# Kernel optimization log

Measured on AMD Instinct MI355X. Metric: run time of the kernel, lower is better.

The kernel has to match this reference:

```python
import jax, jax.numpy as jnp
import numpy as np

DT = 0.01
STEPS = 30
D = 2048


def setup_inputs() -> dict:
    key = jax.random.key(0)
    ks = jax.random.split(key, 7)
    B, S = 4, 4096
    x = jax.random.normal(ks[0], (B, S, D), jnp.float32)
    lorenz = jnp.array([10.0, 28.0, 8.0 / 3.0], jnp.float32)
    strength = jnp.float32(0.3)
    W_in = jax.random.normal(ks[1], (3, D), jnp.float32) / np.sqrt(D)
    b_in = jax.random.normal(ks[2], (3,), jnp.float32) * 0.01
    W_out = jax.random.normal(ks[3], (D, 18), jnp.float32) / np.sqrt(18.0)
    b_out = jax.random.normal(ks[4], (D,), jnp.float32) * 0.01
    return {"x": x, "lorenz": lorenz, "strength": strength,
            "W_in": W_in, "b_in": b_in, "W_out": W_out, "b_out": b_out}


def _deriv(s, sigma, rho, beta):
    xx, yy, zz = s[..., 0], s[..., 1], s[..., 2]
    return jnp.stack([sigma * (yy - xx), xx * (rho - zz) - yy, xx * yy - beta * zz], axis=-1)


def reference(x, lorenz, strength, W_in, b_in, W_out, b_out):
    orig_shape = x.shape
    xf = x.reshape(-1, x.shape[-1])            # [N, D]
    state0 = xf @ W_in.T + b_in                # [N, 3]
    params = jnp.clip(jnp.abs(lorenz), 0.1, None)
    sigma, rho, beta = params[0], params[1], params[2]

    def step(s, _):
        k1 = _deriv(s, sigma, rho, beta)
        k2 = _deriv(s + 0.5 * DT * k1, sigma, rho, beta)
        k3 = _deriv(s + 0.5 * DT * k2, sigma, rho, beta)
        k4 = _deriv(s + DT * k3, sigma, rho, beta)
        s2 = s + (DT / 6.0) * (k1 + 2.0 * k2 + 2.0 * k3 + k4)
        return s2, s2

    _, ys = jax.lax.scan(step, state0, None, length=STEPS)  # [STEPS, N, 3]
    traj = jnp.concatenate([state0[:, None], jnp.moveaxis(ys, 0, 1)], axis=1)  # [N, STEPS+1, 3]

    feats = jnp.concatenate([
        traj[:, 0],                         # initial state
        traj[:, -1],                        # final state
        traj.mean(axis=1),
        traj.std(axis=1, ddof=1),           # torch.std is unbiased by default
        traj.min(axis=1),
        traj.max(axis=1),
    ], axis=-1)                             # [N, 18]

    pert = feats @ W_out.T + b_out          # [N, D]
    out = xf + jnp.tanh(pert) * jnp.abs(strength)
    return out.reshape(orig_shape)
```

## Files before the change

kernel.cpp:

```cpp
#include <hip/hip_runtime.h>
#include <math.h>

#define DD 2048
#define DTC 0.01f
#define NSTEPS 30

typedef float floatx4 __attribute__((ext_vector_type(4)));

__device__ __forceinline__ void lorenz_deriv(float x, float y, float z,
                                             float sigma, float rho, float beta,
                                             float& dx, float& dy, float& dz) {
    dx = sigma * (y - x);
    dy = x * (rho - z) - y;
    dz = x * y - beta * z;
}

__device__ __forceinline__ float fast_tanh(float p) {
    float e = __expf(2.0f * p);
    return 1.0f - __fdividef(2.0f, e + 1.0f);
}

__global__ __launch_bounds__(256) void kA_state0(
    const float* __restrict__ x, const float* __restrict__ W_in,
    const float* __restrict__ b_in, float* __restrict__ state0,
    const float* __restrict__ W_out, float* __restrict__ wsT) {
    __shared__ float g_lds[4][16][13];
    const int tid = threadIdx.x;
    const int lane = tid & 63;
    const int wv = tid >> 6;
    const int row0 = blockIdx.x * 4;
    const int c0 = tid * 8;

    floatx4 xr[4][2];
#pragma unroll
    for (int r = 0; r < 4; ++r) {
        const float* p = x + (size_t)(row0 + r) * DD + c0;
        xr[r][0] = *reinterpret_cast<const floatx4*>(p);
        xr[r][1] = *reinterpret_cast<const floatx4*>(p + 4);
    }
    floatx4 w[3][2];
#pragma unroll
    for (int k = 0; k < 3; ++k) {
        const float* p = W_in + (size_t)k * DD + c0;
        w[k][0] = *reinterpret_cast<const floatx4*>(p);
        w[k][1] = *reinterpret_cast<const floatx4*>(p + 4);
    }

    float s[12];
#pragma unroll
    for (int r = 0; r < 4; ++r) {
#pragma unroll
        for (int k = 0; k < 3; ++k) {
            floatx4 t = xr[r][0] * w[k][0] + xr[r][1] * w[k][1];
            s[r * 3 + k] = (t.x + t.y) + (t.z + t.w);
        }
    }

#pragma unroll
    for (int o = 0; o < 12; ++o) {
        s[o] += __shfl_xor(s[o], 32, 64);
        s[o] += __shfl_xor(s[o], 16, 64);
    }
    if (lane < 16) {
#pragma unroll
        for (int o = 0; o < 12; ++o) g_lds[wv][lane][o] = s[o];
    }
    __syncthreads();

    if (tid < 192) {
        const int o = tid >> 4;
        const int j = tid & 15;
        float v = g_lds[0][j][o] + g_lds[1][j][o] + g_lds[2][j][o] + g_lds[3][j][o];
#pragma unroll
        for (int off = 1; off < 16; off <<= 1) v += __shfl_xor(v, off, 64);
        if (j == 0) {
            state0[(size_t)(row0 + o / 3) * 3 + (o % 3)] = v + b_in[o % 3];
        }
    }

    if (blockIdx.x < 144) {
        const int oidx = blockIdx.x * 256 + tid;
        const int k = oidx >> 11;
        const int c = oidx & 2047;
        wsT[oidx] = W_out[c * 18 + k];
    }
}

__global__ __launch_bounds__(256) void kB_integrate(
    const float* __restrict__ state0, const float* __restrict__ lorenz,
    float* __restrict__ feats) {
    const int row = blockIdx.x * 256 + threadIdx.x;
    const float sigma = fmaxf(fabsf(lorenz[0]), 0.1f);
    const float rho   = fmaxf(fabsf(lorenz[1]), 0.1f);
    const float beta  = fmaxf(fabsf(lorenz[2]), 0.1f);

    float sx = state0[(size_t)row * 3 + 0];
    float sy = state0[(size_t)row * 3 + 1];
    float sz = state0[(size_t)row * 3 + 2];
    const float ix = sx, iy = sy, iz = sz;
    float sux = sx, suy = sy, suz = sz;
    float sqx = sx * sx, sqy = sy * sy, sqz = sz * sz;
    float mnx = sx, mny = sy, mnz = sz;
    float mxx = sx, mxy = sy, mxz = sz;
#pragma unroll 1
    for (int t = 0; t < NSTEPS; ++t) {
        float k1x, k1y, k1z, k2x, k2y, k2z, k3x, k3y, k3z, k4x, k4y, k4z;
        float ax, ay, az;
        lorenz_deriv(sx, sy, sz, sigma, rho, beta, k1x, k1y, k1z);
        ax = sx + 0.5f * DTC * k1x; ay = sy + 0.5f * DTC * k1y; az = sz + 0.5f * DTC * k1z;
        lorenz_deriv(ax, ay, az, sigma, rho, beta, k2x, k2y, k2z);
        ax = sx + 0.5f * DTC * k2x; ay = sy + 0.5f * DTC * k2y; az = sz + 0.5f * DTC * k2z;
        lorenz_deriv(ax, ay, az, sigma, rho, beta, k3x, k3y, k3z);
        ax = sx + DTC * k3x; ay = sy + DTC * k3y; az = sz + DTC * k3z;
        lorenz_deriv(ax, ay, az, sigma, rho, beta, k4x, k4y, k4z);
        sx += (DTC / 6.0f) * (k1x + 2.0f * k2x + 2.0f * k3x + k4x);
        sy += (DTC / 6.0f) * (k1y + 2.0f * k2y + 2.0f * k3y + k4y);
        sz += (DTC / 6.0f) * (k1z + 2.0f * k2z + 2.0f * k3z + k4z);
        sux += sx; suy += sy; suz += sz;
        sqx += sx * sx; sqy += sy * sy; sqz += sz * sz;
        mnx = fminf(mnx, sx); mny = fminf(mny, sy); mnz = fminf(mnz, sz);
        mxx = fmaxf(mxx, sx); mxy = fmaxf(mxy, sy); mxz = fmaxf(mxz, sz);
    }
    const float inv31 = 1.0f / 31.0f;
    const float inv30 = 1.0f / 30.0f;
    const float mex = sux * inv31, mey = suy * inv31, mez = suz * inv31;
    const float vax = fmaxf((sqx - sux * mex) * inv30, 0.0f);
    const float vay = fmaxf((sqy - suy * mey) * inv30, 0.0f);
    const float vaz = fmaxf((sqz - suz * mez) * inv30, 0.0f);
    float* f = feats + (size_t)row * 18;
    f[0]  = ix;  f[1]  = iy;  f[2]  = iz;
    f[3]  = sx;  f[4]  = sy;  f[5]  = sz;
    f[6]  = mex; f[7]  = mey; f[8]  = mez;
    f[9]  = sqrtf(vax); f[10] = sqrtf(vay); f[11] = sqrtf(vaz);
    f[12] = mnx; f[13] = mny; f[14] = mnz;
    f[15] = mxx; f[16] = mxy; f[17] = mxz;
}

__global__ __launch_bounds__(256) void kC_out(
    const float* __restrict__ x, const float* __restrict__ feats,
    const float* __restrict__ wsT, const float* __restrict__ b_out,
    const float* __restrict__ strength, float* __restrict__ out) {
    __shared__ float f_lds[32 * 18];
    const int tid = threadIdx.x;
    const int row0 = blockIdx.x * 32;
    const int c0 = blockIdx.y * 1024 + tid * 4;

    {
        const float* src = feats + (size_t)row0 * 18;
        f_lds[tid] = src[tid];
        f_lds[tid + 256] = src[tid + 256];
        if (tid < 64) f_lds[tid + 512] = src[tid + 512];
    }

    floatx4 wk[18];
#pragma unroll
    for (int k = 0; k < 18; ++k) {
        wk[k] = *reinterpret_cast<const floatx4*>(wsT + (size_t)k * DD + c0);
    }
    const floatx4 bo = *reinterpret_cast<const floatx4*>(b_out + c0);
    const float sabs = fabsf(strength[0]);
    __syncthreads();

#pragma unroll 1
    for (int r = 0; r < 32; r += 2) {
        const int rowA = row0 + r, rowB = row0 + r + 1;
        const float* fA = f_lds + r * 18;
        const float* fB = f_lds + (r + 1) * 18;
        const floatx4 xA = *reinterpret_cast<const floatx4*>(x + (size_t)rowA * DD + c0);
        const floatx4 xB = *reinterpret_cast<const floatx4*>(x + (size_t)rowB * DD + c0);
        floatx4 pA = bo, pB = bo;
#pragma unroll
        for (int k = 0; k < 18; ++k) {
            pA += fA[k] * wk[k];
            pB += fB[k] * wk[k];
        }
        floatx4 oA, oB;
        oA.x = xA.x + fast_tanh(pA.x) * sabs;
        oA.y = xA.y + fast_tanh(pA.y) * sabs;
        oA.z = xA.z + fast_tanh(pA.z) * sabs;
        oA.w = xA.w + fast_tanh(pA.w) * sabs;
        oB.x = xB.x + fast_tanh(pB.x) * sabs;
        oB.y = xB.y + fast_tanh(pB.y) * sabs;
        oB.z = xB.z + fast_tanh(pB.z) * sabs;
        oB.w = xB.w + fast_tanh(pB.w) * sabs;
        __builtin_nontemporal_store(oA, reinterpret_cast<floatx4*>(out + (size_t)rowA * DD + c0));
        __builtin_nontemporal_store(oB, reinterpret_cast<floatx4*>(out + (size_t)rowB * DD + c0));
    }
}

extern "C" void kernel_launch(void* const* d_in, const int* in_sizes, int n_in,
                              void* d_out, int out_size, void* d_ws, size_t ws_size,
                              hipStream_t stream) {
    const float* x        = (const float*)d_in[0];
    const float* lorenz   = (const float*)d_in[1];
    const float* strength = (const float*)d_in[2];
    const float* W_in     = (const float*)d_in[3];
    const float* b_in     = (const float*)d_in[4];
    const float* W_out    = (const float*)d_in[5];
    const float* b_out    = (const float*)d_in[6];
    float* out = (float*)d_out;

    const int N = in_sizes[0] / DD;
    float* state0 = (float*)d_ws;
    float* feats  = state0 + (size_t)N * 3;
    float* wsT    = feats + (size_t)N * 18;

    kA_state0<<<N / 4, 256, 0, stream>>>(x, W_in, b_in, state0, W_out, wsT);
    kB_integrate<<<N / 256, 256, 0, stream>>>(state0, lorenz, feats);
    dim3 g3(N / 32, DD / 1024);
    kC_out<<<g3, 256, 0, stream>>>(x, feats, wsT, b_out, strength, out);
}
```

Baseline: 77.91 us.

## Restructure state0 GEMV to wave-per-4-rows with register-held W_in; move W_out transpose

```diff
diff --git a/kernel.cpp b/kernel.cpp
--- a/kernel.cpp
+++ b/kernel.cpp
@@ -20,76 +20,75 @@
     return 1.0f - __fdividef(2.0f, e + 1.0f);
 }
 
-__global__ __launch_bounds__(256) void kA_state0(
+__global__ __launch_bounds__(256, 3) void kA_state0(
     const float* __restrict__ x, const float* __restrict__ W_in,
-    const float* __restrict__ b_in, float* __restrict__ state0,
-    const float* __restrict__ W_out, float* __restrict__ wsT) {
-    __shared__ float g_lds[4][16][13];
+    const float* __restrict__ b_in, float* __restrict__ state0) {
     const int tid = threadIdx.x;
     const int lane = tid & 63;
     const int wv = tid >> 6;
-    const int row0 = blockIdx.x * 4;
-    const int c0 = tid * 8;
-
-    floatx4 xr[4][2];
-#pragma unroll
-    for (int r = 0; r < 4; ++r) {
-        const float* p = x + (size_t)(row0 + r) * DD + c0;
-        xr[r][0] = *reinterpret_cast<const floatx4*>(p);
-        xr[r][1] = *reinterpret_cast<const floatx4*>(p + 4);
-    }
-    floatx4 w[3][2];
+    const int wave_id = blockIdx.x * 4 + wv;
+    const int r0 = wave_id * 4;
+    const int c = lane * 4;
+
+    const float b0 = b_in[0], b1 = b_in[1], b2 = b_in[2];
+
+    floatx4 w[3][8];
 #pragma unroll
     for (int k = 0; k < 3; ++k) {
-        const float* p = W_in + (size_t)k * DD + c0;
-        w[k][0] = *reinterpret_cast<const floatx4*>(p);
-        w[k][1] = *reinterpret_cast<const floatx4*>(p + 4);
-    }
-
-    float s[12];
-#pragma unroll
-    for (int r = 0; r < 4; ++r) {
-#pragma unroll
-        for (int k = 0; k < 3; ++k) {
-            floatx4 t = xr[r][0] * w[k][0] + xr[r][1] * w[k][1];
-            s[r * 3 + k] = (t.x + t.y) + (t.z + t.w);
-        }
-    }
-
-#pragma unroll
-    for (int o = 0; o < 12; ++o) {
-        s[o] += __shfl_xor(s[o], 32, 64);
-        s[o] += __shfl_xor(s[o], 16, 64);
-    }
-    if (lane < 16) {
-#pragma unroll
-        for (int o = 0; o < 12; ++o) g_lds[wv][lane][o] = s[o];
-    }
-    __syncthreads();
-
-    if (tid < 192) {
-        const int o = tid >> 4;
-        const int j = tid & 15;
-        float v = g_lds[0][j][o] + g_lds[1][j][o] + g_lds[2][j][o] + g_lds[3][j][o];
-#pragma unroll
-        for (int off = 1; off < 16; off <<= 1) v += __shfl_xor(v, off, 64);
-        if (j == 0) {
-            state0[(size_t)(row0 + o / 3) * 3 + (o % 3)] = v + b_in[o % 3];
-        }
-    }
-
-    if (blockIdx.x < 144) {
-        const int oidx = blockIdx.x * 256 + tid;
-        const int k = oidx >> 11;
-        const int c = oidx & 2047;
-        wsT[oidx] = W_out[c * 18 + k];
+        const float* p = W_in + (size_t)k * DD + c;
+#pragma unroll
+        for (int m = 0; m < 8; ++m)
+            w[k][m] = *reinterpret_cast<const floatx4*>(p + m * 256);
+    }
+
+#pragma unroll
+    for (int rr = 0; rr < 4; ++rr) {
+        const int r = r0 + rr;
+        const float* xp = x + (size_t)r * DD + c;
+        floatx4 xv[8];
+#pragma unroll
+        for (int m = 0; m < 8; ++m)
+            xv[m] = *reinterpret_cast<const floatx4*>(xp + m * 256);
+
+        floatx4 a0 = {0.f, 0.f, 0.f, 0.f}, a1 = a0, a2 = a0;
+#pragma unroll
+        for (int m = 0; m < 8; ++m) {
+            a0 += xv[m] * w[0][m];
+            a1 += xv[m] * w[1][m];
+            a2 += xv[m] * w[2][m];
+        }
+        float s0 = (a0.x + a0.y) + (a0.z + a0.w);
+        float s1 = (a1.x + a1.y) + (a1.z + a1.w);
+        float s2 = (a2.x + a2.y) + (a2.z + a2.w);
+#pragma unroll
+        for (int off = 32; off > 0; off >>= 1) {
+            s0 += __shfl_xor(s0, off, 64);
+            s1 += __shfl_xor(s1, off, 64);
+            s2 += __shfl_xor(s2, off, 64);
+        }
+        if (lane == 0) {
+            float* sp = state0 + (size_t)r * 3;
+            sp[0] = s0 + b0;
+            sp[1] = s1 + b1;
+            sp[2] = s2 + b2;
+        }
     }
 }
 
 __global__ __launch_bounds__(256) void kB_integrate(
     const float* __restrict__ state0, const float* __restrict__ lorenz,
-    float* __restrict__ feats) {
-    const int row = blockIdx.x * 256 + threadIdx.x;
+    float* __restrict__ feats,
+    const float* __restrict__ W_out, float* __restrict__ wsT) {
+    const int tid = threadIdx.x;
+#pragma unroll
+    for (int i = 0; i < 3; ++i) {
+        const int oidx = blockIdx.x * 768 + i * 256 + tid;
+        if (oidx < 18 * DD) {
+            wsT[oidx] = W_out[(oidx & 2047) * 18 + (oidx >> 11)];
+        }
+    }
+
+    const int row = blockIdx.x * 256 + tid;
     const float sigma = fmaxf(fabsf(lorenz[0]), 0.1f);
     const float rho   = fmaxf(fabsf(lorenz[1]), 0.1f);
     const float beta  = fmaxf(fabsf(lorenz[2]), 0.1f);
@@ -205,8 +204,8 @@
     float* feats  = state0 + (size_t)N * 3;
     float* wsT    = feats + (size_t)N * 18;
 
-    kA_state0<<<N / 4, 256, 0, stream>>>(x, W_in, b_in, state0, W_out, wsT);
-    kB_integrate<<<N / 256, 256, 0, stream>>>(state0, lorenz, feats);
+    kA_state0<<<N / 16, 256, 0, stream>>>(x, W_in, b_in, state0);
+    kB_integrate<<<N / 256, 256, 0, stream>>>(state0, lorenz, feats, W_out, wsT);
     dim3 g3(N / 32, DD / 1024);
     kC_out<<<g3, 256, 0, stream>>>(x, feats, wsT, b_out, strength, out);
 }
```

After: 81.59 us. 1.05x slower.
